# Kernel optimization log

Measured on AMD Instinct MI355X. Metric: run time of the kernel, lower is better.

The kernel has to match this reference:

```python
import jax, jax.numpy as jnp
import numpy as np

D_MODEL = 1024
NUM_HEADS = 16
D_HEAD = D_MODEL // NUM_HEADS
MAX_SEQ_LEN = 2048
THETA = 10000.0
BATCH = 2
SEQ = 2048


def _rope_tables():
    # inv_freq over even dims; emb interleaves each freq twice: [f0,f0,f1,f1,...]
    inv_freq = 1.0 / (THETA ** (jnp.arange(0, D_HEAD, 2, dtype=jnp.float32) / D_HEAD))
    t = jnp.arange(MAX_SEQ_LEN, dtype=jnp.float32)
    freqs = jnp.einsum('i,j->ij', t, inv_freq)  # [S, d_head/2]
    emb = jnp.stack((freqs, freqs), axis=-1).reshape(MAX_SEQ_LEN, D_HEAD)
    return jnp.cos(emb), jnp.sin(emb)


def _rotate_half(x):
    # pairwise interleaved rotation: (x0,x1,x2,x3,...) -> (-x1,x0,-x3,x2,...)
    xr = x.reshape(x.shape[:-1] + (D_HEAD // 2, 2))
    x1, x2 = xr[..., 0], xr[..., 1]
    return jnp.stack((-x2, x1), axis=-1).reshape(x.shape)


def setup_inputs() -> dict:
    key = jax.random.key(0)
    ks = jax.random.split(key, 5)
    std = np.sqrt(2.0 / (D_MODEL + D_MODEL)).astype(np.float32)
    return {
        'in_features': jax.random.normal(ks[0], (BATCH, SEQ, D_MODEL), dtype=jnp.float32),
        'token_positions': jnp.arange(SEQ, dtype=jnp.int64) if jax.config.jax_enable_x64 else jnp.arange(SEQ, dtype=jnp.int32),
        'wq': jax.random.normal(ks[1], (D_MODEL, D_MODEL), dtype=jnp.float32) * std,
        'wk': jax.random.normal(ks[2], (D_MODEL, D_MODEL), dtype=jnp.float32) * std,
        'wv': jax.random.normal(ks[3], (D_MODEL, D_MODEL), dtype=jnp.float32) * std,
        'wo': jax.random.normal(ks[4], (D_MODEL, D_MODEL), dtype=jnp.float32) * std,
    }


def reference(in_features, token_positions, wq, wk, wv, wo):
    b, s, _ = in_features.shape
    cos_tab, sin_tab = _rope_tables()
    cos = cos_tab[token_positions]  # [s, d_head]
    sin = sin_tab[token_positions]

    def split_heads(t):  # [b, s, d_model] -> [b, h, s, d_head]
        return t.reshape(b, s, NUM_HEADS, D_HEAD).transpose(0, 2, 1, 3)

    q = split_heads(jnp.einsum('bsd,ed->bse', in_features, wq))
    k = split_heads(jnp.einsum('bsd,ed->bse', in_features, wk))
    v = split_heads(jnp.einsum('bsd,ed->bse', in_features, wv))

    q = q * cos + _rotate_half(q) * sin
    k = k * cos + _rotate_half(k) * sin

    scale = 1.0 / np.sqrt(D_HEAD).astype(np.float32)
    scores = jnp.einsum('bhqd,bhkd->bhqk', q, k) * scale  # [b,h,s,s]
    causal = jnp.tril(jnp.ones((s, s), dtype=bool))
    scores = jnp.where(causal, scores, -jnp.inf)
    weights = jax.nn.softmax(scores, axis=-1)
    out = jnp.einsum('bhqk,bhkd->bhqd', weights, v)
    out = out.transpose(0, 2, 1, 3).reshape(b, s, D_MODEL)
    return jnp.einsum('bsd,ed->bse', out, wo)
```

## Files before the change

### kernel.cpp

```cpp
#include <hip/hip_runtime.h>


typedef __attribute__((ext_vector_type(8))) short bf16x8;
typedef __attribute__((ext_vector_type(4))) float f32x4;

__device__ __forceinline__ short f2bf(float f) {
  unsigned u = __float_as_uint(f);
  unsigned r = (u + 0x7fffu + ((u >> 16) & 1u)) >> 16;
  return (short)(r & 0xFFFFu);
}

__device__ __forceinline__ unsigned pk2(float a, float b) {
  return __builtin_amdgcn_perm(__float_as_uint(b) + 0x8000u,
                               __float_as_uint(a) + 0x8000u, 0x07060302u);
}

__device__ __forceinline__ float exp2x(float x) {
  float r;
  asm("v_exp_f32 %0, %1" : "=v"(r) : "v"(x));
  return r;
}

__device__ __forceinline__ void async16(const void* g, void* l) {
  __builtin_amdgcn_global_load_lds(
      (const __attribute__((address_space(1))) void*)g,
      (__attribute__((address_space(3))) void*)l, 16, 0, 0);
}

__device__ __forceinline__ void cstore(short* C, size_t i, float v) { C[i] = f2bf(v); }
__device__ __forceinline__ void cstore(float* C, size_t i, float v) { C[i] = v; }

__global__ void cast_all(const float4* __restrict__ X,
                         const float4* __restrict__ w0, const float4* __restrict__ w1,
                         const float4* __restrict__ w2, const float4* __restrict__ w3,
                         short* __restrict__ Xb, short* __restrict__ Wb) {
  int t = blockIdx.x * 256 + threadIdx.x;
  const float4* s;
  short4* d;
  if (t < (1 << 20)) {
    s = X + t; d = (short4*)Xb + t;
  } else {
    int u = t - (1 << 20);
    int which = u >> 18;
    s = ((which == 0) ? w0 : (which == 1) ? w1 : (which == 2) ? w2 : w3) + (u & 0x3FFFF);
    d = (short4*)Wb + u;
  }
  float4 v = *s;
  *d = make_short4(f2bf(v.x), f2bf(v.y), f2bf(v.z), f2bf(v.w));
}

enum EpiMode { EPI_ROW, EPI_KFRAG, EPI_VFRAG };

template <typename OUT, int MR, int NR, bool ROPE, EpiMode EM, bool MAPB>
__device__ __forceinline__ void gemm_core(short* __restrict__ As, short* __restrict__ Bs,
                                          const short* __restrict__ A, const short* __restrict__ B,
                                          OUT* __restrict__ C, int bm, int bn, int ldc,
                                          const int* __restrict__ pos) {
  constexpr int BM = 32 * MR, BN = 32 * NR;
  constexpr int NLD = (BM * 4 + BN * 4) / 256;
  const int tid  = threadIdx.x;
  const int lane = tid & 63, wave = tid >> 6;
  const int col  = lane & 15, quad = lane >> 4;
  const int wm = (wave & 1) * (16 * MR), wn = (wave >> 1) * (16 * NR);

  f32x4 acc[MR][NR];
#pragma unroll
  for (int i = 0; i < MR; i++)
#pragma unroll
    for (int j = 0; j < NR; j++) acc[i][j] = (f32x4){0.f, 0.f, 0.f, 0.f};

  auto stage = [&](int k0, int bu) {
#pragma unroll
    for (int c = tid; c < BM * 4; c += 256) {
      int r = c >> 2, cc = (c & 3) << 3;
      async16(A + (size_t)(bm + r) * 1024 + k0 + cc, As + bu * BM * 32 + c * 8);
    }
#pragma unroll
    for (int c = tid; c < BN * 4; c += 256) {
      int r = c >> 2, cc = (c & 3) << 3;
      int rg = bn + r;
      if (MAPB) {
        int k6 = rg & 63;
        rg = (rg & ~63) | ((k6 < 32) ? (k6 << 1) : (((k6 - 32) << 1) | 1));
      }
      async16(B + (size_t)rg * 1024 + k0 + cc, Bs + bu * BN * 32 + c * 8);
    }
  };

  stage(0, 0);
  stage(32, 1);
  if constexpr (NLD == 4) asm volatile("s_waitcnt vmcnt(4)" ::: "memory");
  else                    asm volatile("s_waitcnt vmcnt(3)" ::: "memory");
  __builtin_amdgcn_s_barrier();

  int cur = 0, nxt = 2;
  for (int it = 0; it < 32; ++it) {
    if (it < 30) stage((it + 2) * 32, nxt);
    const short* as = As + cur * (BM * 32);
    const short* bs = Bs + cur * (BN * 32);

    bf16x8 af[MR], bfr[NR];
#pragma unroll
    for (int i = 0; i < MR; i++)
      af[i] = *(const bf16x8*)(as + (wm + i * 16 + col) * 32 + quad * 8);
#pragma unroll
    for (int i = 0; i < NR; i++)
      bfr[i] = *(const bf16x8*)(bs + (wn + i * 16 + col) * 32 + quad * 8);
#pragma unroll
    for (int mi = 0; mi < MR; mi++)
#pragma unroll
      for (int ni = 0; ni < NR; ni++)
        acc[mi][ni] = __builtin_amdgcn_mfma_f32_16x16x32_bf16(af[mi], bfr[ni], acc[mi][ni], 0, 0, 0);

    if (it < 30) {
      if constexpr (NLD == 4) asm volatile("s_waitcnt vmcnt(4)" ::: "memory");
      else                    asm volatile("s_waitcnt vmcnt(3)" ::: "memory");
    } else {
      asm volatile("s_waitcnt vmcnt(0)" ::: "memory");
    }
    __builtin_amdgcn_s_barrier();
    cur = (cur == 2) ? 0 : cur + 1;
    nxt = (nxt == 2) ? 0 : nxt + 1;
  }

  if (ROPE) {
    float invf[2];
#pragma unroll
    for (int ni = 0; ni < 2; ni++) {
      int p = ni * 16 + col;
      invf[ni] = exp2f(-0.4152410118609203f * (float)p) * 0.15915494309189535f;
    }
#pragma unroll
    for (int mi = 0; mi < MR; mi++) {
#pragma unroll
      for (int r = 0; r < 4; r++) {
        int row = bm + wm + mi * 16 + quad * 4 + r;
        float fp = (float)pos[row & 2047];
#pragma unroll
        for (int ni = 0; ni < 2; ni++) {
          float rev = fp * invf[ni];
          rev -= floorf(rev);
          float sn = __builtin_amdgcn_sinf(rev);
          float cs = __builtin_amdgcn_cosf(rev);
          float x  = acc[mi][ni][r];
          float yv = acc[mi][ni + 2][r];
          acc[mi][ni][r]     = fmaf(x, cs, -yv * sn);
          acc[mi][ni + 2][r] = fmaf(yv, cs, x * sn);
        }
      }
    }
  }

  if (EM == EPI_ROW) {
#pragma unroll
    for (int mi = 0; mi < MR; mi++) {
#pragma unroll
      for (int r = 0; r < 4; r++) {
        size_t row = (size_t)(bm + wm + mi * 16 + quad * 4 + r);
#pragma unroll
        for (int ni = 0; ni < NR; ni++) {
          int cg = bn + wn + ni * 16 + col;
          cstore(C, row * ldc + cg, acc[mi][ni][r]);
        }
      }
    }
  } else if (EM == EPI_KFRAG) {
#pragma unroll
    for (int mi = 0; mi < MR; mi++) {
#pragma unroll
      for (int r = 0; r < 4; r++) {
        int m = bm + wm + mi * 16 + quad * 4 + r;
        int bq = m >> 11, key = m & 2047;
        int kt = key >> 6, nb = (key >> 4) & 3, cl = key & 15;
#pragma unroll
        for (int ni = 0; ni < NR; ni++) {
          int e = bn + wn + ni * 16 + col;
          int h = e >> 6, d = e & 63;
          size_t seg = ((((size_t)(bq * 16 + h) * 32 + kt) * 4 + nb) * 2 + (d >> 5));
          cstore((short*)C, seg * 512 + (((d >> 3) & 3) * 16 + cl) * 8 + (d & 7), acc[mi][ni][r]);
        }
      }
    }
  } else {
#pragma unroll
    for (int mi = 0; mi < MR; mi++) {
#pragma unroll
      for (int r = 0; r < 4; r++) {
        int e = bm + wm + mi * 16 + quad * 4 + r;
        int h = e >> 6, d = e & 63;
        int nb = d >> 4, cl = d & 15;
#pragma unroll
        for (int ni = 0; ni < NR; ni++) {
          int m = bn + wn + ni * 16 + col;
          int bq = m >> 11, key = m & 2047;
          int kt = key >> 6, k64 = key & 63;
          size_t seg = ((((size_t)(bq * 16 + h) * 32 + kt) * 4 + nb) * 2 + (k64 >> 5));
          cstore((short*)C, seg * 512 + (((k64 >> 3) & 3) * 16 + cl) * 8 + (k64 & 7), acc[mi][ni][r]);
        }
      }
    }
  }
}

__device__ __forceinline__ void gemm_qk(short* __restrict__ As, short* __restrict__ Bqs,
                                        short* __restrict__ Bks,
                                        const short* __restrict__ A,
                                        const short* __restrict__ Bq,
                                        const short* __restrict__ Bk,
                                        short* __restrict__ Qo, short* __restrict__ Kf,
                                        int bm, int bn, const int* __restrict__ pos) {
  const int tid  = threadIdx.x;
  const int lane = tid & 63, wave = tid >> 6;
  const int col  = lane & 15, quad = lane >> 4;
  const int wm = (wave & 1) * 64, wn = (wave >> 1) * 64;

  f32x4 aq[4][4], ak[4][4];
#pragma unroll
  for (int i = 0; i < 4; i++)
#pragma unroll
    for (int j = 0; j < 4; j++) {
      aq[i][j] = (f32x4){0.f, 0.f, 0.f, 0.f};
      ak[i][j] = (f32x4){0.f, 0.f, 0.f, 0.f};
    }

  auto stage = [&](int k0, int bu) {
#pragma unroll
    for (int c = tid; c < 512; c += 256) {
      int r = c >> 2, cc = (c & 3) << 3;
      async16(A + (size_t)(bm + r) * 1024 + k0 + cc, As + bu * 4096 + c * 8);
    }
#pragma unroll
    for (int c = tid; c < 512; c += 256) {
      int r = c >> 2, cc = (c & 3) << 3;
      int rg = bn + r;
      int k6 = rg & 63;
      rg = (rg & ~63) | ((k6 < 32) ? (k6 << 1) : (((k6 - 32) << 1) | 1));
      async16(Bq + (size_t)rg * 1024 + k0 + cc, Bqs + bu * 4096 + c * 8);
      async16(Bk + (size_t)rg * 1024 + k0 + cc, Bks + bu * 4096 + c * 8);
    }
  };

  stage(0, 0);
  stage(32, 1);
  asm volatile("s_waitcnt vmcnt(6)" ::: "memory");
  __builtin_amdgcn_s_barrier();

  int cur = 0, nxt = 2;
  for (int it = 0; it < 32; ++it) {
    if (it < 30) stage((it + 2) * 32, nxt);
    const short* as = As + cur * 4096;
    const short* bq = Bqs + cur * 4096;
    const short* bk = Bks + cur * 4096;

    bf16x8 af[4], bfq[4], bfk[4];
#pragma unroll
    for (int i = 0; i < 4; i++)
      af[i] = *(const bf16x8*)(as + (wm + i * 16 + col) * 32 + quad * 8);
#pragma unroll
    for (int i = 0; i < 4; i++) {
      bfq[i] = *(const bf16x8*)(bq + (wn + i * 16 + col) * 32 + quad * 8);
      bfk[i] = *(const bf16x8*)(bk + (wn + i * 16 + col) * 32 + quad * 8);
    }
#pragma unroll
    for (int mi = 0; mi < 4; mi++)
#pragma unroll
      for (int ni = 0; ni < 4; ni++) {
        aq[mi][ni] = __builtin_amdgcn_mfma_f32_16x16x32_bf16(af[mi], bfq[ni], aq[mi][ni], 0, 0, 0);
        ak[mi][ni] = __builtin_amdgcn_mfma_f32_16x16x32_bf16(af[mi], bfk[ni], ak[mi][ni], 0, 0, 0);
      }

    if (it < 30) asm volatile("s_waitcnt vmcnt(6)" ::: "memory");
    else         asm volatile("s_waitcnt vmcnt(0)" ::: "memory");
    __builtin_amdgcn_s_barrier();
    cur = (cur == 2) ? 0 : cur + 1;
    nxt = (nxt == 2) ? 0 : nxt + 1;
  }

  float invf[2];
#pragma unroll
  for (int ni = 0; ni < 2; ni++) {
    int p = ni * 16 + col;
    invf[ni] = exp2f(-0.4152410118609203f * (float)p) * 0.15915494309189535f;
  }
#pragma unroll
  for (int mi = 0; mi < 4; mi++) {
#pragma unroll
    for (int r = 0; r < 4; r++) {
      int row = bm + wm + mi * 16 + quad * 4 + r;
      float fp = (float)pos[row & 2047];
#pragma unroll
      for (int ni = 0; ni < 2; ni++) {
        float rev = fp * invf[ni];
        rev -= floorf(rev);
        float sn = __builtin_amdgcn_sinf(rev);
        float cs = __builtin_amdgcn_cosf(rev);
        float xq = aq[mi][ni][r], yq = aq[mi][ni + 2][r];
        aq[mi][ni][r]     = fmaf(xq, cs, -yq * sn);
        aq[mi][ni + 2][r] = fmaf(yq, cs, xq * sn);
        float xk = ak[mi][ni][r], yk = ak[mi][ni + 2][r];
        ak[mi][ni][r]     = fmaf(xk, cs, -yk * sn);
        ak[mi][ni + 2][r] = fmaf(yk, cs, xk * sn);
      }
    }
  }

#pragma unroll
  for (int mi = 0; mi < 4; mi++) {
#pragma unroll
    for (int r = 0; r < 4; r++) {
      size_t row = (size_t)(bm + wm + mi * 16 + quad * 4 + r);
#pragma unroll
      for (int ni = 0; ni < 4; ni++) {
        int cg = bn + wn + ni * 16 + col;
        Qo[row * 1024 + cg] = f2bf(aq[mi][ni][r]);
      }
    }
  }
#pragma unroll
  for (int mi = 0; mi < 4; mi++) {
#pragma unroll
    for (int r = 0; r < 4; r++) {
      int m = bm + wm + mi * 16 + quad * 4 + r;
      int bq2 = m >> 11, key = m & 2047;
      int kt = key >> 6, nb = (key >> 4) & 3, cl = key & 15;
#pragma unroll
      for (int ni = 0; ni < 4; ni++) {
        int e = bn + wn + ni * 16 + col;
        int h = e >> 6, d = e & 63;
        size_t seg = ((((size_t)(bq2 * 16 + h) * 32 + kt) * 4 + nb) * 2 + (d >> 5));
        Kf[seg * 512 + (((d >> 3) & 3) * 16 + cl) * 8 + (d & 7)] = f2bf(ak[mi][ni][r]);
      }
    }
  }
}

__global__ __launch_bounds__(256, 2) void qkv_gemm(const short* __restrict__ Xb,
                                                   const short* __restrict__ Wq,
                                                   const short* __restrict__ Wk,
                                                   const short* __restrict__ Wv,
                                                   short* __restrict__ Qo,
                                                   short* __restrict__ Kf,
                                                   short* __restrict__ Vf,
                                                   const int* __restrict__ pos) {
  __shared__ __align__(16) short sm[3 * 4096 * 3];
  if (blockIdx.z == 0)
    gemm_qk(sm, sm + 12288, sm + 24576, Xb, Wq, Wk, Qo, Kf,
            blockIdx.x * 128, blockIdx.y * 128, pos);
  else
    gemm_core<short, 4, 4, false, EPI_VFRAG, false>(sm, sm + 12288, Wv, Xb, Vf,
                                                    blockIdx.y * 128, blockIdx.x * 128, 0, pos);
}

__global__ __launch_bounds__(256) void out_gemm(const short* __restrict__ Ctx,
                                                const short* __restrict__ Wo,
                                                float* __restrict__ C) {
  __shared__ __align__(16) short sm[3 * 64 * 32 + 3 * 128 * 32];
  gemm_core<float, 2, 4, false, EPI_ROW, false>(sm, sm + 3 * 64 * 32, Ctx, Wo, C,
                                                blockIdx.x * 64, blockIdx.y * 128, 1024, nullptr);
}

__global__ __launch_bounds__(256, 3) void flash_attn(const short* __restrict__ Q,
                                                     const short* __restrict__ Kf,
                                                     const short* __restrict__ Vf,
                                                     short* __restrict__ ctx) {
  const int y = blockIdx.y;
  const int g = y >> 3, r8 = y & 7;
  const int qt = (g == 0) ? 31 - r8 : (g == 1) ? r8 : (g == 2) ? 23 - r8 : 8 + r8;
  const int bh = blockIdx.x;
  const int b = bh >> 4, h = bh & 15;
  __shared__ __align__(16) short Ps[4][16 * 72];
  __shared__ __align__(16) short Ksm[2][4096];
  __shared__ __align__(16) short Vsm[2][4096];
  const int tid = threadIdx.x, lane = tid & 63, wave = tid >> 6;
  const int col = lane & 15, quad = lane >> 4;

  const short* Kg = Kf + (size_t)bh * 131072;
  const short* Vg = Vf + (size_t)bh * 131072;

  const float C1 = 0.18033688011112042f;
  const float mC2 = -17.31234049066756f;

  short* myPs = &Ps[wave][0];
  const int cx = col & 3;
  const int pswr0 = col * 72 + ((0 ^ cx) << 4) + quad * 4;
  const int pswr1 = col * 72 + ((1 ^ cx) << 4) + quad * 4;
  const int pswr2 = col * 72 + ((2 ^ cx) << 4) + quad * 4;
  const int pswr3 = col * 72 + ((3 ^ cx) << 4) + quad * 4;
  const int psrd0 = col * 72 + (((quad >> 1) ^ cx) << 4) + (quad & 1) * 8;
  const int psrd1 = col * 72 + ((((quad >> 1) + 2) ^ cx) << 4) + (quad & 1) * 8;

  auto stageKV = [&](int kt, short* kb, short* vb) {
    const short* kg = Kg + kt * 4096;
    const short* vg = Vg + kt * 4096;
#pragma unroll
    for (int c = tid; c < 512; c += 256) {
      async16(kg + c * 8, kb + c * 8);
      async16(vg + c * 8, vb + c * 8);
    }
  };

  const size_t qrow = (size_t)(b * 2048 + qt * 64 + wave * 16 + col);
  bf16x8 qf0 = *(const bf16x8*)(Q + qrow * 1024 + h * 64 + quad * 8);
  bf16x8 qf1 = *(const bf16x8*)(Q + qrow * 1024 + h * 64 + 32 + quad * 8);

  float l_i = 0.f;
  f32x4 o_acc[4];
#pragma unroll
  for (int i = 0; i < 4; i++) o_acc[i] = (f32x4){0.f, 0.f, 0.f, 0.f};

  short *kcur = &Ksm[0][0], *vcur = &Vsm[0][0];
  short *knxt = &Ksm[1][0], *vnxt = &Vsm[1][0];

  stageKV(0, kcur, vcur);
  asm volatile("s_waitcnt vmcnt(0)" ::: "memory");
  __builtin_amdgcn_s_barrier();

  bf16x8 afp0 = (bf16x8){0,0,0,0,0,0,0,0}, afp1 = (bf16x8){0,0,0,0,0,0,0,0};
  bf16x8 vfp[4][2];
#pragma unroll
  for (int i = 0; i < 4; i++) vfp[i][0] = vfp[i][1] = (bf16x8){0,0,0,0,0,0,0,0};

  for (int kt = 0; kt < qt; ++kt) {
    stageKV(kt + 1, knxt, vnxt);

    bf16x8 kfr[4][2];
#pragma unroll
    for (int nb = 0; nb < 4; nb++) {
      kfr[nb][0] = *(const bf16x8*)(kcur + (nb * 2 + 0) * 512 + lane * 8);
      kfr[nb][1] = *(const bf16x8*)(kcur + (nb * 2 + 1) * 512 + lane * 8);
    }

    f32x4 s_acc[4];
    __builtin_amdgcn_s_setprio(1);
#pragma unroll
    for (int nb = 0; nb < 4; nb++) {
      f32x4 z = (f32x4){0.f, 0.f, 0.f, 0.f};
      z = __builtin_amdgcn_mfma_f32_16x16x32_bf16(kfr[nb][0], qf0, z, 0, 0, 0);
      z = __builtin_amdgcn_mfma_f32_16x16x32_bf16(kfr[nb][1], qf1, z, 0, 0, 0);
      s_acc[nb] = z;
    }
    if (kt > 0) {
#pragma unroll
      for (int nb = 0; nb < 4; nb++) {
        o_acc[nb] = __builtin_amdgcn_mfma_f32_16x16x32_bf16(afp0, vfp[nb][0], o_acc[nb], 0, 0, 0);
        o_acc[nb] = __builtin_amdgcn_mfma_f32_16x16x32_bf16(afp1, vfp[nb][1], o_acc[nb], 0, 0, 0);
      }
    }
    __builtin_amdgcn_s_setprio(0);

#pragma unroll
    for (int nb = 0; nb < 4; nb++) {
      vfp[nb][0] = *(const bf16x8*)(vcur + (nb * 2 + 0) * 512 + lane * 8);
      vfp[nb][1] = *(const bf16x8*)(vcur + (nb * 2 + 1) * 512 + lane * 8);
    }

#pragma unroll
    for (int nb = 0; nb < 4; nb++) {
      float p0 = exp2x(fmaf(s_acc[nb][0], C1, mC2));
      float p1 = exp2x(fmaf(s_acc[nb][1], C1, mC2));
      float p2 = exp2x(fmaf(s_acc[nb][2], C1, mC2));
      float p3 = exp2x(fmaf(s_acc[nb][3], C1, mC2));
      int wr = (nb == 0) ? pswr0 : (nb == 1) ? pswr1 : (nb == 2) ? pswr2 : pswr3;
      *(uint2*)(myPs + wr) = make_uint2(pk2(p0, p1), pk2(p2, p3));
      l_i += (p0 + p1) + (p2 + p3);
    }
    afp0 = *(const bf16x8*)(myPs + psrd0);
    afp1 = *(const bf16x8*)(myPs + psrd1);

    asm volatile("s_waitcnt vmcnt(0)" ::: "memory");
    __builtin_amdgcn_s_barrier();
    short* t;
    t = kcur; kcur = knxt; knxt = t;
    t = vcur; vcur = vnxt; vnxt = t;
  }

  {
    const int ql = wave * 16 + col;
    const int kl = quad * 4;

    bf16x8 kfr[4][2];
#pragma unroll
    for (int nb = 0; nb < 4; nb++) {
      kfr[nb][0] = *(const bf16x8*)(kcur + (nb * 2 + 0) * 512 + lane * 8);
      kfr[nb][1] = *(const bf16x8*)(kcur + (nb * 2 + 1) * 512 + lane * 8);
    }

    f32x4 s_acc[4];
    __builtin_amdgcn_s_setprio(1);
#pragma unroll
    for (int nb = 0; nb < 4; nb++) {
      f32x4 z = (f32x4){0.f, 0.f, 0.f, 0.f};
      z = __builtin_amdgcn_mfma_f32_16x16x32_bf16(kfr[nb][0], qf0, z, 0, 0, 0);
      z = __builtin_amdgcn_mfma_f32_16x16x32_bf16(kfr[nb][1], qf1, z, 0, 0, 0);
      s_acc[nb] = z;
    }
    if (qt > 0) {
#pragma unroll
      for (int nb = 0; nb < 4; nb++) {
        o_acc[nb] = __builtin_amdgcn_mfma_f32_16x16x32_bf16(afp0, vfp[nb][0], o_acc[nb], 0, 0, 0);
        o_acc[nb] = __builtin_amdgcn_mfma_f32_16x16x32_bf16(afp1, vfp[nb][1], o_acc[nb], 0, 0, 0);
      }
    }
    __builtin_amdgcn_s_setprio(0);

#pragma unroll
    for (int nb = 0; nb < 4; nb++) {
      vfp[nb][0] = *(const bf16x8*)(vcur + (nb * 2 + 0) * 512 + lane * 8);
      vfp[nb][1] = *(const bf16x8*)(vcur + (nb * 2 + 1) * 512 + lane * 8);
    }

#pragma unroll
    for (int nb = 0; nb < 4; nb++) {
      float pv[4];
#pragma unroll
      for (int r = 0; r < 4; r++) {
        pv[r] = exp2x(fmaf(s_acc[nb][r], C1, mC2));
        if ((nb * 16 + kl + r) > ql) pv[r] = 0.f;
      }
      int wr = (nb == 0) ? pswr0 : (nb == 1) ? pswr1 : (nb == 2) ? pswr2 : pswr3;
      *(uint2*)(myPs + wr) = make_uint2(pk2(pv[0], pv[1]), pk2(pv[2], pv[3]));
      l_i += (pv[0] + pv[1]) + (pv[2] + pv[3]);
    }
    afp0 = *(const bf16x8*)(myPs + psrd0);
    afp1 = *(const bf16x8*)(myPs + psrd1);

    __builtin_amdgcn_s_setprio(1);
#pragma unroll
    for (int nb = 0; nb < 4; nb++) {
      o_acc[nb] = __builtin_amdgcn_mfma_f32_16x16x32_bf16(afp0, vfp[nb][0], o_acc[nb], 0, 0, 0);
      o_acc[nb] = __builtin_amdgcn_mfma_f32_16x16x32_bf16(afp1, vfp[nb][1], o_acc[nb], 0, 0, 0);
    }
    __builtin_amdgcn_s_setprio(0);
  }

  l_i += __shfl_xor(l_i, 16);
  l_i += __shfl_xor(l_i, 32);
  float invl = 1.0f / l_i;

#pragma unroll
  for (int r = 0; r < 4; r++) {
    float inv = __shfl(invl, quad * 4 + r);
    size_t row = (size_t)(b * 2048 + qt * 64 + wave * 16 + quad * 4 + r);
#pragma unroll
    for (int nb = 0; nb < 4; nb++)
      ctx[row * 1024 + h * 64 + nb * 16 + col] = f2bf(o_acc[nb][r] * inv);
  }
}

extern "C" void kernel_launch(void* const* d_in, const int* in_sizes, int n_in,
                              void* d_out, int out_size, void* d_ws, size_t ws_size,
                              hipStream_t stream) {
  const float* X  = (const float*)d_in[0];
  const int* pos  = (const int*)d_in[1];
  const float* wq = (const float*)d_in[2];
  const float* wk = (const float*)d_in[3];
  const float* wv = (const float*)d_in[4];
  const float* wo = (const float*)d_in[5];
  float* out = (float*)d_out;

  short* Xb  = (short*)d_ws;
  short* Wqb = Xb + (1 << 22);
  short* Wkb = Wqb + (1 << 20);
  short* Wvb = Wkb + (1 << 20);
  short* Wob = Wvb + (1 << 20);
  short* Qb  = Wob + (1 << 20);
  short* Kfb = Qb + (1 << 22);
  short* Vfb = Kfb + (1 << 22);
  short* Ctx = Vfb + (1 << 22);

  cast_all<<<8192, 256, 0, stream>>>((const float4*)X, (const float4*)wq, (const float4*)wk,
                                     (const float4*)wv, (const float4*)wo, Xb, Wqb);
  qkv_gemm<<<dim3(32, 8, 2), 256, 0, stream>>>(Xb, Wqb, Wkb, Wvb, Qb, Kfb, Vfb, pos);
  flash_attn<<<dim3(32, 32), 256, 0, stream>>>(Qb, Kfb, Vfb, Ctx);
  out_gemm<<<dim3(64, 8), 256, 0, stream>>>(Ctx, Wob, out);
}
```

Before: 164.4 us.

## Fuse V projection into Q/K GEMM and enlarge out-projection tiles

Before, the Q/K/V projection kernel ran separate blocks for Q+K and for V, so the X tile was loaded twice. Now one block computes all three projections from a single staged X tile, with a third accumulator set and packed vectorised stores into the V fragment layout. The grid shrinks from 512 to 256 blocks and occupancy drops to one block per CU, since register and LDS use grow. The output GEMM also moves from 64x128 to 128x128 tiles, which halves its grid to 256 blocks.

```diff
diff --git a/kernel.cpp b/kernel.cpp
--- a/kernel.cpp
+++ b/kernel.cpp
@@ -8,6 +8,10 @@
   unsigned u = __float_as_uint(f);
   unsigned r = (u + 0x7fffu + ((u >> 16) & 1u)) >> 16;
   return (short)(r & 0xFFFFu);
+}
+
+__device__ __forceinline__ unsigned pk2rne(float a, float b) {
+  return ((unsigned)(unsigned short)f2bf(b) << 16) | (unsigned short)f2bf(a);
 }
 
 __device__ __forceinline__ unsigned pk2(float a, float b) {
@@ -164,85 +168,60 @@
         }
       }
     }
-  } else if (EM == EPI_KFRAG) {
-#pragma unroll
-    for (int mi = 0; mi < MR; mi++) {
-#pragma unroll
-      for (int r = 0; r < 4; r++) {
-        int m = bm + wm + mi * 16 + quad * 4 + r;
-        int bq = m >> 11, key = m & 2047;
-        int kt = key >> 6, nb = (key >> 4) & 3, cl = key & 15;
-#pragma unroll
-        for (int ni = 0; ni < NR; ni++) {
-          int e = bn + wn + ni * 16 + col;
-          int h = e >> 6, d = e & 63;
-          size_t seg = ((((size_t)(bq * 16 + h) * 32 + kt) * 4 + nb) * 2 + (d >> 5));
-          cstore((short*)C, seg * 512 + (((d >> 3) & 3) * 16 + cl) * 8 + (d & 7), acc[mi][ni][r]);
-        }
-      }
-    }
-  } else {
-#pragma unroll
-    for (int mi = 0; mi < MR; mi++) {
-#pragma unroll
-      for (int r = 0; r < 4; r++) {
-        int e = bm + wm + mi * 16 + quad * 4 + r;
-        int h = e >> 6, d = e & 63;
-        int nb = d >> 4, cl = d & 15;
-#pragma unroll
-        for (int ni = 0; ni < NR; ni++) {
-          int m = bn + wn + ni * 16 + col;
-          int bq = m >> 11, key = m & 2047;
-          int kt = key >> 6, k64 = key & 63;
-          size_t seg = ((((size_t)(bq * 16 + h) * 32 + kt) * 4 + nb) * 2 + (k64 >> 5));
-          cstore((short*)C, seg * 512 + (((k64 >> 3) & 3) * 16 + cl) * 8 + (k64 & 7), acc[mi][ni][r]);
-        }
-      }
-    }
-  }
-}
-
-__device__ __forceinline__ void gemm_qk(short* __restrict__ As, short* __restrict__ Bqs,
-                                        short* __restrict__ Bks,
-                                        const short* __restrict__ A,
-                                        const short* __restrict__ Bq,
-                                        const short* __restrict__ Bk,
-                                        short* __restrict__ Qo, short* __restrict__ Kf,
-                                        int bm, int bn, const int* __restrict__ pos) {
+  }
+}
+
+__global__ __launch_bounds__(256, 1) void qkv_gemm(const short* __restrict__ Xb,
+                                                   const short* __restrict__ Wq,
+                                                   const short* __restrict__ Wk,
+                                                   const short* __restrict__ Wv,
+                                                   short* __restrict__ Qo,
+                                                   short* __restrict__ Kf,
+                                                   short* __restrict__ Vf,
+                                                   const int* __restrict__ pos) {
+  __shared__ __align__(16) short sm[49152];
+  short* As  = sm;
+  short* Bqs = sm + 12288;
+  short* Bks = sm + 24576;
+  short* Bvs = sm + 36864;
+
+  const int bm = blockIdx.x * 128, bn = blockIdx.y * 128;
   const int tid  = threadIdx.x;
   const int lane = tid & 63, wave = tid >> 6;
   const int col  = lane & 15, quad = lane >> 4;
   const int wm = (wave & 1) * 64, wn = (wave >> 1) * 64;
 
-  f32x4 aq[4][4], ak[4][4];
+  f32x4 aq[4][4], ak[4][4], av[4][4];
 #pragma unroll
   for (int i = 0; i < 4; i++)
 #pragma unroll
     for (int j = 0; j < 4; j++) {
       aq[i][j] = (f32x4){0.f, 0.f, 0.f, 0.f};
       ak[i][j] = (f32x4){0.f, 0.f, 0.f, 0.f};
+      av[i][j] = (f32x4){0.f, 0.f, 0.f, 0.f};
     }
 
   auto stage = [&](int k0, int bu) {
 #pragma unroll
     for (int c = tid; c < 512; c += 256) {
       int r = c >> 2, cc = (c & 3) << 3;
-      async16(A + (size_t)(bm + r) * 1024 + k0 + cc, As + bu * 4096 + c * 8);
+      async16(Xb + (size_t)(bm + r) * 1024 + k0 + cc, As + bu * 4096 + c * 8);
     }
 #pragma unroll
     for (int c = tid; c < 512; c += 256) {
       int r = c >> 2, cc = (c & 3) << 3;
       int rg = bn + r;
       int k6 = rg & 63;
-      rg = (rg & ~63) | ((k6 < 32) ? (k6 << 1) : (((k6 - 32) << 1) | 1));
-      async16(Bq + (size_t)rg * 1024 + k0 + cc, Bqs + bu * 4096 + c * 8);
-      async16(Bk + (size_t)rg * 1024 + k0 + cc, Bks + bu * 4096 + c * 8);
+      int rp = (rg & ~63) | ((k6 < 32) ? (k6 << 1) : (((k6 - 32) << 1) | 1));
+      async16(Wq + (size_t)rp * 1024 + k0 + cc, Bqs + bu * 4096 + c * 8);
+      async16(Wk + (size_t)rp * 1024 + k0 + cc, Bks + bu * 4096 + c * 8);
+      async16(Wv + (size_t)rg * 1024 + k0 + cc, Bvs + bu * 4096 + c * 8);
     }
   };
 
   stage(0, 0);
   stage(32, 1);
-  asm volatile("s_waitcnt vmcnt(6)" ::: "memory");
+  asm volatile("s_waitcnt vmcnt(8)" ::: "memory");
   __builtin_amdgcn_s_barrier();
 
   int cur = 0, nxt = 2;
@@ -251,8 +230,9 @@
     const short* as = As + cur * 4096;
     const short* bq = Bqs + cur * 4096;
     const short* bk = Bks + cur * 4096;
-
-    bf16x8 af[4], bfq[4], bfk[4];
+    const short* bv = Bvs + cur * 4096;
+
+    bf16x8 af[4], bfq[4], bfk[4], bfv[4];
 #pragma unroll
     for (int i = 0; i < 4; i++)
       af[i] = *(const bf16x8*)(as + (wm + i * 16 + col) * 32 + quad * 8);
@@ -260,6 +240,7 @@
     for (int i = 0; i < 4; i++) {
       bfq[i] = *(const bf16x8*)(bq + (wn + i * 16 + col) * 32 + quad * 8);
       bfk[i] = *(const bf16x8*)(bk + (wn + i * 16 + col) * 32 + quad * 8);
+      bfv[i] = *(const bf16x8*)(bv + (wn + i * 16 + col) * 32 + quad * 8);
     }
 #pragma unroll
     for (int mi = 0; mi < 4; mi++)
@@ -267,9 +248,10 @@
       for (int ni = 0; ni < 4; ni++) {
         aq[mi][ni] = __builtin_amdgcn_mfma_f32_16x16x32_bf16(af[mi], bfq[ni], aq[mi][ni], 0, 0, 0);
         ak[mi][ni] = __builtin_amdgcn_mfma_f32_16x16x32_bf16(af[mi], bfk[ni], ak[mi][ni], 0, 0, 0);
-      }
-
-    if (it < 30) asm volatile("s_waitcnt vmcnt(6)" ::: "memory");
+        av[mi][ni] = __builtin_amdgcn_mfma_f32_16x16x32_bf16(af[mi], bfv[ni], av[mi][ni], 0, 0, 0);
+      }
+
+    if (it < 30) asm volatile("s_waitcnt vmcnt(8)" ::: "memory");
     else         asm volatile("s_waitcnt vmcnt(0)" ::: "memory");
     __builtin_amdgcn_s_barrier();
     cur = (cur == 2) ? 0 : cur + 1;
@@ -332,31 +314,35 @@
       }
     }
   }
-}
-
-__global__ __launch_bounds__(256, 2) void qkv_gemm(const short* __restrict__ Xb,
-                                                   const short* __restrict__ Wq,
-                                                   const short* __restrict__ Wk,
-                                                   const short* __restrict__ Wv,
-                                                   short* __restrict__ Qo,
-                                                   short* __restrict__ Kf,
-                                                   short* __restrict__ Vf,
-                                                   const int* __restrict__ pos) {
-  __shared__ __align__(16) short sm[3 * 4096 * 3];
-  if (blockIdx.z == 0)
-    gemm_qk(sm, sm + 12288, sm + 24576, Xb, Wq, Wk, Qo, Kf,
-            blockIdx.x * 128, blockIdx.y * 128, pos);
-  else
-    gemm_core<short, 4, 4, false, EPI_VFRAG, false>(sm, sm + 12288, Wv, Xb, Vf,
-                                                    blockIdx.y * 128, blockIdx.x * 128, 0, pos);
+  {
+    const int k7base = (quad & 1) * 4;
+#pragma unroll
+    for (int mi = 0; mi < 4; mi++) {
+      int m0 = bm + wm + mi * 16 + quad * 4;
+      int bq2 = m0 >> 11, key = m0 & 2047;
+      int kt = key >> 6;
+      int k16 = (mi * 2 + (quad >> 1)) & 3;
+      int half = mi >> 1;
+#pragma unroll
+      for (int ni = 0; ni < 4; ni++) {
+        int e = bn + wn + ni * 16 + col;
+        int h = e >> 6, d = e & 63;
+        int nb = d >> 4, cl = d & 15;
+        size_t seg = ((((size_t)(bq2 * 16 + h) * 32 + kt) * 4 + nb) * 2 + half);
+        size_t off = seg * 512 + (size_t)(k16 * 16 + cl) * 8 + k7base;
+        *(uint2*)(Vf + off) = make_uint2(pk2rne(av[mi][ni][0], av[mi][ni][1]),
+                                         pk2rne(av[mi][ni][2], av[mi][ni][3]));
+      }
+    }
+  }
 }
 
 __global__ __launch_bounds__(256) void out_gemm(const short* __restrict__ Ctx,
                                                 const short* __restrict__ Wo,
                                                 float* __restrict__ C) {
-  __shared__ __align__(16) short sm[3 * 64 * 32 + 3 * 128 * 32];
-  gemm_core<float, 2, 4, false, EPI_ROW, false>(sm, sm + 3 * 64 * 32, Ctx, Wo, C,
-                                                blockIdx.x * 64, blockIdx.y * 128, 1024, nullptr);
+  __shared__ __align__(16) short sm[3 * 128 * 32 + 3 * 128 * 32];
+  gemm_core<float, 4, 4, false, EPI_ROW, false>(sm, sm + 3 * 128 * 32, Ctx, Wo, C,
+                                                blockIdx.x * 128, blockIdx.y * 128, 1024, nullptr);
 }
 
 __global__ __launch_bounds__(256, 3) void flash_attn(const short* __restrict__ Q,
@@ -570,7 +556,7 @@
 
   cast_all<<<8192, 256, 0, stream>>>((const float4*)X, (const float4*)wq, (const float4*)wk,
                                      (const float4*)wv, (const float4*)wo, Xb, Wqb);
-  qkv_gemm<<<dim3(32, 8, 2), 256, 0, stream>>>(Xb, Wqb, Wkb, Wvb, Qb, Kfb, Vfb, pos);
+  qkv_gemm<<<dim3(32, 8), 256, 0, stream>>>(Xb, Wqb, Wkb, Wvb, Qb, Kfb, Vfb, pos);
   flash_attn<<<dim3(32, 32), 256, 0, stream>>>(Qb, Kfb, Vfb, Ctx);
-  out_gemm<<<dim3(64, 8), 256, 0, stream>>>(Ctx, Wob, out);
-}
+  out_gemm<<<dim3(32, 8), 256, 0, stream>>>(Ctx, Wob, out);
+}
```

After: 168.8 us. 2.7% more time.
